# Kernel tuning notes

Hardware: AMD Instinct MI355X
Metric: run time of the kernel (lower is better)

The kernel has to match this reference:

```python
import jax, jax.numpy as jnp
import numpy as np

V = 100000   # nodes (atoms)
E = 400000   # directed edges (bonds x2)
N = 74       # node_feat_size
NE = 12      # edge_feat_size
G = 200      # graph_feat_size
L = 2        # num_layers - 1 GNN layers
OUT = 1      # output_size
NG = 4000    # molecules in the batch


def _lin_init(k, fan_in, fan_out):
    s = 1.0 / np.sqrt(fan_in)
    return jax.random.uniform(k, (fan_in, fan_out), jnp.float32, -s, s)


def setup_inputs() -> dict:
    key = jax.random.key(0)
    ks = list(jax.random.split(key, 40))
    p = {}
    # node feats uniform in (0.05, 0.95) so mask = 1/(sum(h[:,-4:])*(1-h[:,0])) - 1 is finite
    p["node_feats"] = jax.random.uniform(ks[0], (V, N), jnp.float32, 0.05, 0.95)
    p["edge_feats"] = jax.random.normal(ks[1], (E, NE), jnp.float32)
    # GetContext params
    p["pn_W"] = _lin_init(ks[2], N, G);            p["pn_b"] = jnp.zeros((G,), jnp.float32)
    p["pe1_W"] = _lin_init(ks[3], N + NE, G);      p["pe1_b"] = jnp.zeros((G,), jnp.float32)
    p["pe2_W"] = _lin_init(ks[4], 2 * G, 1);       p["pe2_b"] = jnp.zeros((1,), jnp.float32)
    p["et_W"] = _lin_init(ks[5], G, G);            p["et_b"] = jnp.zeros((G,), jnp.float32)
    p["gru0_Wih"] = _lin_init(ks[6], G, 3 * G);    p["gru0_Whh"] = _lin_init(ks[7], G, 3 * G)
    p["gru0_bih"] = jnp.zeros((3 * G,), jnp.float32)
    p["gru0_bhh"] = jnp.zeros((3 * G,), jnp.float32)
    # stacked GNNLayer params
    p["gnn_pe_W"] = jnp.stack([_lin_init(ks[8 + l], 2 * G, 1) for l in range(L)])
    p["gnn_pe_b"] = jnp.zeros((L, 1), jnp.float32)
    p["gnn_pn_W"] = jnp.stack([_lin_init(ks[10 + l], G, G) for l in range(L)])
    p["gnn_pn_b"] = jnp.zeros((L, G), jnp.float32)
    p["gnn_gru_Wih"] = jnp.stack([_lin_init(ks[12 + l], G, 3 * G) for l in range(L)])
    p["gnn_gru_Whh"] = jnp.stack([_lin_init(ks[14 + l], G, 3 * G) for l in range(L)])
    p["gnn_gru_bih"] = jnp.zeros((L, 3 * G), jnp.float32)
    p["gnn_gru_bhh"] = jnp.zeros((L, 3 * G), jnp.float32)
    p["pred_W"] = _lin_init(ks[16], G, OUT);       p["pred_b"] = jnp.zeros((OUT,), jnp.float32)
    # graph structure
    p["src"] = jax.random.randint(ks[17], (E,), 0, V)
    p["dst"] = jax.random.randint(ks[18], (E,), 0, V)
    p["graph_ids"] = jnp.arange(V, dtype=jnp.int32) // (V // NG)  # sorted, balanced, non-empty
    p["n_graphs"] = NG
    return p


def _edge_softmax(logits, dst, num_nodes):
    # softmax over incoming edges of each destination node (DGL edge_softmax)
    m = jax.ops.segment_max(logits, dst, num_segments=num_nodes)
    e = jnp.exp(logits - m[dst])
    s = jax.ops.segment_sum(e, dst, num_segments=num_nodes)
    return e / s[dst]


def _gru_cell(x, h, Wih, Whh, bih, bhh):
    gi = x @ Wih + bih
    gh = h @ Whh + bhh
    ir, iz, inn = jnp.split(gi, 3, axis=-1)
    hr, hz, hn = jnp.split(gh, 3, axis=-1)
    r = jax.nn.sigmoid(ir + hr)
    z = jax.nn.sigmoid(iz + hz)
    n = jnp.tanh(inn + r * hn)
    return (1.0 - z) * n + z * h


def _forward(node_feats, edge_feats, pn_W, pn_b, pe1_W, pe1_b, pe2_W, pe2_b,
             et_W, et_b, gru0_Wih, gru0_Whh, gru0_bih, gru0_bhh,
             gnn_pe_W, gnn_pe_b, gnn_pn_W, gnn_pn_b,
             gnn_gru_Wih, gnn_gru_Whh, gnn_gru_bih, gnn_gru_bhh,
             pred_W, pred_b, src, dst, graph_ids, n_graphs):
    Vn = node_feats.shape[0]
    lrelu = jax.nn.leaky_relu  # slope 0.01, matches torch default
    # mask from original node features g.ndata['h']
    mask = jnp.sum(node_feats[:, -4:], axis=1) * (1.0 - node_feats[:, 0])
    mask = 1.0 / mask - 1.0
    # --- GetContext ---
    hv_new = lrelu(node_feats @ pn_W + pn_b)                               # (V, G)
    he1 = lrelu(jnp.concatenate([node_feats[src], edge_feats], 1) @ pe1_W + pe1_b)  # (E, G)
    he2 = jnp.concatenate([hv_new[dst], he1], 1)                           # (E, 2G)
    logits = lrelu(he2 @ pe2_W + pe2_b)                                    # (E, 1)
    a = _edge_softmax(logits, dst, Vn)
    e = a * (he1 @ et_W + et_b)                                            # (E, G)
    c = jax.ops.segment_sum(e, dst, num_segments=Vn)                       # (V, G)
    nf = jax.nn.relu(_gru_cell(jax.nn.elu(c), hv_new,
                               gru0_Wih, gru0_Whh, gru0_bih, gru0_bhh))
    # --- GNN layers ---
    for l in range(gnn_pe_W.shape[0]):
        he = jnp.concatenate([nf[dst], nf[src]], 1)                        # (E, 2G)
        lg = lrelu(he @ gnn_pe_W[l] + gnn_pe_b[l])                         # (E, 1)
        a = _edge_softmax(lg, dst, Vn)
        hvp = nf @ gnn_pn_W[l] + gnn_pn_b[l]                               # (V, G)
        c = jax.ops.segment_sum(hvp[src] * a, dst, num_segments=Vn)        # (V, G)
        nf = jax.nn.relu(_gru_cell(jax.nn.elu(c), nf,
                                   gnn_gru_Wih[l], gnn_gru_Whh[l],
                                   gnn_gru_bih[l], gnn_gru_bhh[l]))
    # --- readout ---
    atom_pka = nf @ pred_W + pred_b                                        # (V, 1)
    atom_pka = -(atom_pka + mask[:, None])
    h_pow = jnp.power(10.0, atom_pka)
    g_feats = -jnp.log10(jax.ops.segment_sum(h_pow, graph_ids, num_segments=n_graphs))
    atom_pka_out = -atom_pka
    return g_feats, atom_pka_out


def reference(node_feats, edge_feats, pn_W, pn_b, pe1_W, pe1_b, pe2_W, pe2_b,
              et_W, et_b, gru0_Wih, gru0_Whh, gru0_bih, gru0_bhh,
              gnn_pe_W, gnn_pe_b, gnn_pn_W, gnn_pn_b,
              gnn_gru_Wih, gnn_gru_Whh, gnn_gru_bih, gnn_gru_bhh,
              pred_W, pred_b, src, dst, graph_ids, n_graphs):
    return _forward(node_feats, edge_feats, pn_W, pn_b, pe1_W, pe1_b, pe2_W, pe2_b,
                    et_W, et_b, gru0_Wih, gru0_Whh, gru0_bih, gru0_bhh,
                    gnn_pe_W, gnn_pe_b, gnn_pn_W, gnn_pn_b,
                    gnn_gru_Wih, gnn_gru_Whh, gnn_gru_bih, gnn_gru_bhh,
                    pred_W, pred_b, src, dst, graph_ids, n_graphs)
```

## Files before the change

kernel.cpp:

```cpp
#include <hip/hip_runtime.h>
#include <hip/hip_bf16.h>
#include <math.h>

#define V_N    100000
#define E_N    400000
#define NFEAT  74
#define NEFEAT 12
#define G_DIM  200
#define LDA    224
#define L_N    2
#define NG_N   4000
#define NROWB  391
#define NROWP  392
#define NSWZ   (NROWP / 8 * 56)
#define NSWZG  (NROWP / 8 * 112)

static inline int cdiv(int a, int b) { return (a + b - 1) / b; }

__device__ __forceinline__ float lrelu_f(float x) { return x > 0.f ? x : 0.01f * x; }
__device__ __forceinline__ float sigmoid_f(float x) { return 1.f / (1.f + expf(-x)); }
__device__ __forceinline__ float elu_f(float x) { return x > 0.f ? x : expm1f(x); }
__device__ __forceinline__ float bf2f(__hip_bfloat16 x) { return __bfloat162float(x); }
__device__ __forceinline__ float bfbits2f(short s) {
    return __uint_as_float(((unsigned)(unsigned short)s) << 16);
}

__device__ __forceinline__ short f2bf(float f) {
    __hip_bfloat16 b = __float2bfloat16(f);
    short s;
    __builtin_memcpy(&s, &b, 2);
    return s;
}

typedef short short8 __attribute__((ext_vector_type(8)));
typedef short short4v __attribute__((ext_vector_type(4)));
typedef float f32x4 __attribute__((ext_vector_type(4)));

#define MFMA16(a, b, c) __builtin_amdgcn_mfma_f32_16x16x32_bf16((a), (b), (c), 0, 0, 0)

#define GLOAD_LDS16(gp, lp) \
    __builtin_amdgcn_global_load_lds((const __attribute__((address_space(1))) void*)(gp), \
                                     (__attribute__((address_space(3))) void*)(lp), 16, 0, 0)

__device__ __forceinline__ void swz_decode7(int lin, int& rowBlk, int& cb)
{
    int grp = lin / 56;
    int rem = lin % 56;
    cb = rem >> 3;
    rowBlk = grp * 8 + (rem & 7);
}

__device__ __forceinline__ void swz_decode14(int lin, int& rowBlk, int& cb)
{
    int grp = lin / 112;
    int rem = lin % 112;
    cb = rem >> 3;
    rowBlk = grp * 8 + (rem & 7);
}

__device__ __forceinline__ f32x4 qcalc(const f32x4* wef, f32x4 ef0, f32x4 ef1, f32x4 ef2)
{
    f32x4 q = ef0[0] * wef[0];
    q += ef0[1] * wef[1];
    q += ef0[2] * wef[2];
    q += ef0[3] * wef[3];
    q += ef1[0] * wef[4];
    q += ef1[1] * wef[5];
    q += ef1[2] * wef[6];
    q += ef1[3] * wef[7];
    q += ef2[0] * wef[8];
    q += ef2[1] * wef[9];
    q += ef2[2] * wef[10];
    q += ef2[3] * wef[11];
    return q;
}

__global__ __launch_bounds__(256)
void fill_kernel(float* __restrict__ p, float v, int n)
{
    int i = blockIdx.x * blockDim.x + threadIdx.x;
    if (i < n) p[i] = v;
}

__global__ __launch_bounds__(256)
void fill_int_kernel(int* __restrict__ p, int v, int n)
{
    int i = blockIdx.x * blockDim.x + threadIdx.x;
    if (i < n) p[i] = v;
}

__global__ __launch_bounds__(256)
void pad_zero_kernel(short* __restrict__ base, size_t VP)
{
    int idx = blockIdx.x * blockDim.x + threadIdx.x;
    if (idx >= 4 * V_N) return;
    int mat = idx / V_N, row = idx % V_N;
    short* p = base + (size_t)mat * VP + (long)row * LDA + G_DIM;
    short8 z = {};
    *(short8*)(p) = z;
    *(short8*)(p + 8) = z;
    *(short8*)(p + 16) = z;
}

__global__ __launch_bounds__(256)
void wprep_kernel(const float* __restrict__ W, short* __restrict__ Wp, int K, int Kpad)
{
    int idx = blockIdx.x * 256 + threadIdx.x;
    if (idx >= 256 * Kpad) return;
    int j = idx / Kpad, k = idx % Kpad;
    float v = (j < G_DIM && k < K) ? W[(long)k * G_DIM + j] : 0.f;
    Wp[idx] = f2bf(v);
}

__global__ __launch_bounds__(256)
void wprep_tiled_kernel(const float* __restrict__ W, short* __restrict__ Wp)
{
    int idx = blockIdx.x * 256 + threadIdx.x;
    if (idx >= 7 * 7 * 1024) return;
    int cb = idx / (7 * 1024);
    int r = idx % (7 * 1024);
    int st = r / 1024;
    int r2 = r % 1024;
    int cc = r2 / 32, kk = r2 % 32;
    int col = cb * 32 + cc, k = st * 32 + kk;
    float v = (col < G_DIM && k < G_DIM) ? W[(long)k * G_DIM + col] : 0.f;
    Wp[idx] = f2bf(v);
}

__global__ __launch_bounds__(256)
void gru_wprep_kernel(const float* __restrict__ Wih, const float* __restrict__ Whh,
                      short* __restrict__ Wp)
{
    int idx = blockIdx.x * 256 + threadIdx.x;
    if (idx >= 14 * 14 * 1536) return;
    int cb = idx / (14 * 1536);
    int r = idx % (14 * 1536);
    int st = r / 1536;
    int r2 = r % 1536;
    int g = r2 / 512;
    int r3 = r2 % 512;
    int cc = r3 / 32, kk = r3 % 32;
    int col = cb * 16 + cc;
    float v = 0.f;
    if (col < G_DIM) {
        if (st < 7) {
            int k = st * 32 + kk;
            if (k < G_DIM) v = Wih[(long)k * (3 * G_DIM) + g * G_DIM + col];
        } else {
            int k = (st - 7) * 32 + kk;
            if (k < G_DIM) v = Whh[(long)k * (3 * G_DIM) + g * G_DIM + col];
        }
    }
    Wp[idx] = f2bf(v);
}

__global__ __launch_bounds__(256)
void hist_kernel(const int* __restrict__ dst, int* __restrict__ deg)
{
    int e = blockIdx.x * blockDim.x + threadIdx.x;
    if (e >= E_N) return;
    atomicAdd(&deg[dst[e]], 1);
}

__global__ __launch_bounds__(256)
void scan1_kernel(const int* __restrict__ deg, int* __restrict__ rp, int* __restrict__ bsum)
{
    __shared__ int s[256];
    int tid = threadIdx.x;
    int v = blockIdx.x * 256 + tid;
    int x = (v < V_N) ? deg[v] : 0;
    s[tid] = x;
    __syncthreads();
    for (int off = 1; off < 256; off <<= 1) {
        int t = (tid >= off) ? s[tid - off] : 0;
        __syncthreads();
        s[tid] += t;
        __syncthreads();
    }
    if (v < V_N) rp[v] = s[tid] - x;
    if (tid == 255) bsum[blockIdx.x] = s[255];
}

__global__ void scan2_kernel(int* __restrict__ bsum, int* __restrict__ rp, int nb)
{
    if (threadIdx.x != 0 || blockIdx.x != 0) return;
    int acc = 0;
    for (int b = 0; b < nb; b++) { int t = bsum[b]; bsum[b] = acc; acc += t; }
    rp[V_N] = acc;
}

__global__ __launch_bounds__(256)
void scan3_kernel(int* __restrict__ rp, const int* __restrict__ bsum)
{
    int v = blockIdx.x * 256 + threadIdx.x;
    if (v < V_N) rp[v] += bsum[v >> 8];
}

__global__ __launch_bounds__(256)
void csr_fill_kernel(const int* __restrict__ dst, const int* __restrict__ rp,
                     int* __restrict__ cnt, int* __restrict__ perm)
{
    int e = blockIdx.x * blockDim.x + threadIdx.x;
    if (e >= E_N) return;
    int d = dst[e];
    int pos = rp[d] + atomicAdd(&cnt[d], 1);
    perm[pos] = e;
}

__global__ __launch_bounds__(256)
void gemm_f32a_dual_kernel(const float* __restrict__ Af32,
                           const short* __restrict__ Wp1, const float* __restrict__ b1,
                           const short* __restrict__ Wp2, const float* __restrict__ b2,
                           __hip_bfloat16* __restrict__ C1,
                           __hip_bfloat16* __restrict__ C2)
{
    __shared__ short As[64 * 40];
    __shared__ short Bs1[64 * 40];
    __shared__ short Bs2[64 * 40];
    const int tid = threadIdx.x;
    const int lane = tid & 63;
    const int w = tid >> 6;
    const int quad = lane >> 4;
    const int lm = lane & 15;
    const int rowBase = blockIdx.y * 64;
    const int j0 = blockIdx.x * 64;
    const int arow = tid >> 2;
    const int akc = (tid & 3) * 8;
    const int agrow = rowBase + arow;

    f32x4 acc1[4] = {}, acc2[4] = {};

    for (int k0 = 0; k0 < 96; k0 += 32) {
        short8 av = {};
        if (agrow < V_N) {
            int gk = k0 + akc;
            #pragma unroll
            for (int i = 0; i < 8; i++) {
                int kg = gk + i;
                av[i] = (kg < NFEAT) ? f2bf(Af32[(long)agrow * NFEAT + kg]) : (short)0;
            }
        }
        *(short8*)&As[arow * 40 + akc] = av;
        {
            int col = tid >> 2;
            *(short8*)&Bs1[col * 40 + akc] =
                *(const short8*)(Wp1 + (long)(j0 + col) * 96 + k0 + akc);
            *(short8*)&Bs2[col * 40 + akc] =
                *(const short8*)(Wp2 + (long)(j0 + col) * 96 + k0 + akc);
        }
        __syncthreads();
        short8 a = *(short8*)&As[(w * 16 + lm) * 40 + quad * 8];
        #pragma unroll
        for (int nt = 0; nt < 4; nt++) {
            short8 bb1 = *(short8*)&Bs1[(nt * 16 + lm) * 40 + quad * 8];
            short8 bb2 = *(short8*)&Bs2[(nt * 16 + lm) * 40 + quad * 8];
            acc1[nt] = MFMA16(a, bb1, acc1[nt]);
            acc2[nt] = MFMA16(a, bb2, acc2[nt]);
        }
        __syncthreads();
    }

    #pragma unroll
    for (int nt = 0; nt < 4; nt++) {
        int col = j0 + nt * 16 + lm;
        if (col >= G_DIM) continue;
        float bv1 = b1[col], bv2 = b2[col];
        #pragma unroll
        for (int r = 0; r < 4; r++) {
            int grow = rowBase + w * 16 + quad * 4 + r;
            if (grow >= V_N) continue;
            C1[(long)grow * LDA + col] = __float2bfloat16(lrelu_f(acc1[nt][r] + bv1));
            C2[(long)grow * LDA + col] = __float2bfloat16(acc2[nt][r] + bv2);
        }
    }
}

template<int EPI>
__global__ __launch_bounds__(256)
void gemm_bf16a_kernel(const __hip_bfloat16* __restrict__ Abf,
                       const short* __restrict__ Wp,
                       const float* __restrict__ bias,
                       __hip_bfloat16* __restrict__ Cbf)
{
    __shared__ short As[2][256 * 32];
    __shared__ short Bs[2][32 * 32];
    int rowBlk, cb;
    swz_decode7(blockIdx.x, rowBlk, cb);
    if (rowBlk >= NROWB) return;
    const int tid = threadIdx.x;
    const int lane = tid & 63;
    const int w = tid >> 6;
    const int quad = lane >> 4;
    const int lm = lane & 15;
    const int j0 = cb * 32;
    const int rowBase = rowBlk * 256;

    const short* WpB = Wp + (long)cb * (7 * 1024);
    const short* As_g = (const short*)Abf;
    const long aoff = (long)(rowBase + w * 64 + (lane >> 2)) * LDA + (lane & 3) * 8;
    const int boff = w * 512 + lane * 8;

    auto stage = [&](int st, int buf) {
        const int kl = st * 32;
        #pragma unroll
        for (int c = 0; c < 4; c++)
            GLOAD_LDS16(As_g + aoff + (long)c * 16 * LDA + kl,
                        &As[buf][(w * 64 + c * 16) * 32]);
        if (w < 2)
            GLOAD_LDS16(WpB + st * 1024 + boff, &Bs[buf][w * 512]);
    };

    f32x4 acc[4][2] = {};

    stage(0, 0);
    __syncthreads();

    int buf = 0;
    #pragma unroll 1
    for (int st = 0; st < 7; st++) {
        if (st + 1 < 7) stage(st + 1, buf ^ 1);
        short8 b0 = *(short8*)&Bs[buf][(0 * 16 + lm) * 32 + quad * 8];
        short8 b1 = *(short8*)&Bs[buf][(1 * 16 + lm) * 32 + quad * 8];
        #pragma unroll
        for (int rt = 0; rt < 4; rt++) {
            short8 a = *(short8*)&As[buf][(w * 64 + rt * 16 + lm) * 32 + quad * 8];
            acc[rt][0] = MFMA16(a, b0, acc[rt][0]);
            acc[rt][1] = MFMA16(a, b1, acc[rt][1]);
        }
        __syncthreads();
        buf ^= 1;
    }

    #pragma unroll
    for (int nt = 0; nt < 2; nt++) {
        int col = j0 + nt * 16 + lm;
        if (col >= G_DIM) continue;
        float bv = bias[col];
        #pragma unroll
        for (int rt = 0; rt < 4; rt++) {
            #pragma unroll
            for (int r = 0; r < 4; r++) {
                int grow = rowBase + w * 64 + rt * 16 + quad * 4 + r;
                if (grow >= V_N) continue;
                float v = acc[rt][nt][r] + bv;
                if (EPI == 3) v = elu_f(v);
                Cbf[(long)grow * LDA + col] = __float2bfloat16(v);
            }
        }
    }
}

__global__ __launch_bounds__(256, 3)
void gru_mfma_kernel(const __hip_bfloat16* __restrict__ xc,
                     const __hip_bfloat16* __restrict__ h,
                     const short* __restrict__ Wp,
                     const float* __restrict__ bih, const float* __restrict__ bhh,
                     __hip_bfloat16* __restrict__ out)
{
    __shared__ short As[2][256 * 32];
    __shared__ short Bs[2][3 * 16 * 32];
    int rowBlk, cb;
    swz_decode14(blockIdx.x, rowBlk, cb);
    if (rowBlk >= NROWB) return;
    const int tid = threadIdx.x;
    const int lane = tid & 63;
    const int w = tid >> 6;
    const int quad = lane >> 4;
    const int lm = lane & 15;
    const int j0 = cb * 16;
    const int rowBase = rowBlk * 256;

    const short* WpB = Wp + (long)cb * (14 * 1536);
    const short* xc_s = (const short*)xc;
    const short* h_s = (const short*)h;
    const long aoff = (long)(rowBase + w * 64 + (lane >> 2)) * LDA + (lane & 3) * 8;
    const int boff = w * 512 + lane * 8;

    auto stage = [&](int st, int buf) {
        const short* Ap = (st < 7) ? xc_s : h_s;
        const int kl = (st < 7 ? st : st - 7) * 32;
        #pragma unroll
        for (int c = 0; c < 4; c++)
            GLOAD_LDS16(Ap + aoff + (long)c * 16 * LDA + kl,
                        &As[buf][(w * 64 + c * 16) * 32]);
        if (w < 3)
            GLOAD_LDS16(WpB + st * 1536 + boff, &Bs[buf][w * 512]);
    };

    f32x4 aR[4] = {}, aZ[4] = {}, aNl[4] = {}, aNh[4] = {};

    stage(0, 0);
    __syncthreads();

    int buf = 0;
    #pragma unroll 1
    for (int st = 0; st < 14; st++) {
        if (st + 1 < 14) stage(st + 1, buf ^ 1);
        short8 br = *(short8*)&Bs[buf][(0 * 16 + lm) * 32 + quad * 8];
        short8 bz = *(short8*)&Bs[buf][(1 * 16 + lm) * 32 + quad * 8];
        short8 bn = *(short8*)&Bs[buf][(2 * 16 + lm) * 32 + quad * 8];
        #pragma unroll
        for (int rt = 0; rt < 4; rt++) {
            short8 a = *(short8*)&As[buf][(w * 64 + rt * 16 + lm) * 32 + quad * 8];
            aR[rt] = MFMA16(a, br, aR[rt]);
            aZ[rt] = MFMA16(a, bz, aZ[rt]);
            if (st < 7) aNl[rt] = MFMA16(a, bn, aNl[rt]);
            else        aNh[rt] = MFMA16(a, bn, aNh[rt]);
        }
        __syncthreads();
        buf ^= 1;
    }

    int col = j0 + lm;
    if (col < G_DIM) {
        float b_ir = bih[col], b_iz = bih[G_DIM + col], b_in = bih[2 * G_DIM + col];
        float b_hr = bhh[col], b_hz = bhh[G_DIM + col], b_hn = bhh[2 * G_DIM + col];
        #pragma unroll
        for (int rt = 0; rt < 4; rt++) {
            #pragma unroll
            for (int r = 0; r < 4; r++) {
                int grow = rowBase + w * 64 + rt * 16 + quad * 4 + r;
                if (grow >= V_N) continue;
                float sr = aR[rt][r] + b_ir + b_hr;
                float sz = aZ[rt][r] + b_iz + b_hz;
                float gin = aNl[rt][r] + b_in;
                float ghn = aNh[rt][r] + b_hn;
                float rr = sigmoid_f(sr);
                float zz = sigmoid_f(sz);
                float nn = tanhf(gin + rr * ghn);
                float hval = bf2f(h[(long)grow * LDA + col]);
                float o = (1.f - zz) * nn + zz * hval;
                out[(long)grow * LDA + col] = __float2bfloat16(o > 0.f ? o : 0.f);
            }
        }
    }
}

__global__ __launch_bounds__(256)
void node_dot2_kernel(const __hip_bfloat16* __restrict__ X,
                      const float* __restrict__ wa, const float* __restrict__ wb,
                      float* __restrict__ s1, float* __restrict__ s2)
{
    int w = threadIdx.x >> 6, lane = threadIdx.x & 63;
    int v = blockIdx.x * 4 + w;
    if (v >= V_N) return;
    int vlane = (lane < 50) ? lane : 0;
    short4v pv = *(const short4v*)((const short*)X + (long)v * LDA + vlane * 4);
    f32x4 wav = *(const f32x4*)(wa + vlane * 4);
    float a = 0.f, b = 0.f;
    #pragma unroll
    for (int u = 0; u < 4; u++) a += bfbits2f(pv[u]) * wav[u];
    if (wb) {
        f32x4 wbv = *(const f32x4*)(wb + vlane * 4);
        #pragma unroll
        for (int u = 0; u < 4; u++) b += bfbits2f(pv[u]) * wbv[u];
    }
    if (lane >= 50) { a = 0.f; b = 0.f; }
    for (int off = 32; off > 0; off >>= 1) {
        a += __shfl_down(a, off, 64);
        if (wb) b += __shfl_down(b, off, 64);
    }
    if (lane == 0) {
        s1[v] = a;
        if (wb) s2[v] = b;
    }
}

__global__ __launch_bounds__(256)
void ctx_fused_kernel(const __hip_bfloat16* __restrict__ P,
                      const float* __restrict__ efeat,
                      const int* __restrict__ src,
                      const int* __restrict__ rp, const int* __restrict__ perm,
                      const float* __restrict__ s1,
                      const float* __restrict__ pe1W,
                      const float* __restrict__ pe2W, const float* __restrict__ pe2b,
                      __hip_bfloat16* __restrict__ hbar)
{
    const int tid = threadIdx.x;
    const int w = tid >> 6, lane = tid & 63;
    const int vlane = (lane < 50) ? lane : 0;
    const int v = __builtin_amdgcn_readfirstlane(blockIdx.x * 4 + w);
    if (v >= V_N) return;
    const int b = __builtin_amdgcn_readfirstlane(rp[v]);
    const int en = __builtin_amdgcn_readfirstlane(rp[v + 1]);
    if (en == b) {
        if (lane < 50) {
            short4v z = {};
            *(short4v*)((short*)hbar + (long)v * LDA + lane * 4) = z;
        }
        return;
    }
    f32x4 wef[12];
    #pragma unroll
    for (int j = 0; j < 12; j++)
        wef[j] = *(const f32x4*)(pe1W + (long)(NFEAT + j) * G_DIM + vlane * 4);
    const f32x4 w2 = *(const f32x4*)(pe2W + G_DIM + vlane * 4);
    const float s1b = s1[v] + pe2b[0];

    float m = -INFINITY, ssum = 0.f;
    f32x4 a = {};
    for (int i = b; i < en; i++) {
        const int e = __builtin_amdgcn_readfirstlane(perm[i]);
        const int sN = __builtin_amdgcn_readfirstlane(src[e]);
        const f32x4 ef0 = *(const f32x4*)(efeat + (long)e * NEFEAT);
        const f32x4 ef1 = *(const f32x4*)(efeat + (long)e * NEFEAT + 4);
        const f32x4 ef2 = *(const f32x4*)(efeat + (long)e * NEFEAT + 8);
        const short4v pv = *(const short4v*)((const short*)P + (long)sN * LDA + vlane * 4);
        const f32x4 q = qcalc(wef, ef0, ef1, ef2);
        f32x4 he;
        #pragma unroll
        for (int u = 0; u < 4; u++) he[u] = lrelu_f(bfbits2f(pv[u]) + q[u]);
        float dot = he[0] * w2[0] + he[1] * w2[1] + he[2] * w2[2] + he[3] * w2[3];
        if (lane >= 50) dot = 0.f;
        #pragma unroll
        for (int off = 32; off > 0; off >>= 1) dot += __shfl_xor(dot, off, 64);
        const float l = lrelu_f(dot + s1b);
        if (l <= m) {
            const float wgt = expf(l - m);
            ssum += wgt;
            #pragma unroll
            for (int u = 0; u < 4; u++) a[u] += wgt * he[u];
        } else {
            const float scale = expf(m - l);
            ssum = ssum * scale + 1.f;
            #pragma unroll
            for (int u = 0; u < 4; u++) a[u] = a[u] * scale + he[u];
            m = l;
        }
    }
    const float inv = 1.f / ssum;
    if (lane < 50) {
        short4v o;
        #pragma unroll
        for (int u = 0; u < 4; u++) o[u] = f2bf(a[u] * inv);
        *(short4v*)((short*)hbar + (long)v * LDA + lane * 4) = o;
    }
}

__global__ __launch_bounds__(256)
void gnn_fused_agg_kernel(const __hip_bfloat16* __restrict__ X,
                          const int* __restrict__ src,
                          const int* __restrict__ rp, const int* __restrict__ perm,
                          const float* __restrict__ s1, const float* __restrict__ s2,
                          const float* __restrict__ bias,
                          __hip_bfloat16* __restrict__ out)
{
    const int tid = threadIdx.x;
    const int w = tid >> 6, lane = tid & 63;
    const int vlane = (lane < 50) ? lane : 0;
    const int v = __builtin_amdgcn_readfirstlane(blockIdx.x * 4 + w);
    if (v >= V_N) return;
    const int b = __builtin_amdgcn_readfirstlane(rp[v]);
    const int en = __builtin_amdgcn_readfirstlane(rp[v + 1]);
    if (en == b) {
        if (lane < 50) {
            short4v z = {};
            *(short4v*)((short*)out + (long)v * LDA + lane * 4) = z;
        }
        return;
    }
    const float s1v = s1[v] + bias[0];
    float m = -INFINITY;
    for (int i = b; i < en; i++) {
        const int e = __builtin_amdgcn_readfirstlane(perm[i]);
        const int sN = __builtin_amdgcn_readfirstlane(src[e]);
        m = fmaxf(m, lrelu_f(s1v + s2[sN]));
    }
    f32x4 a = {};
    float ssum = 0.f;
    for (int i = b; i < en; i++) {
        const int e = __builtin_amdgcn_readfirstlane(perm[i]);
        const int sN = __builtin_amdgcn_readfirstlane(src[e]);
        const float l = lrelu_f(s1v + s2[sN]);
        const float wgt = expf(l - m);
        ssum += wgt;
        const short4v pv = *(const short4v*)((const short*)X + (long)sN * LDA + vlane * 4);
        #pragma unroll
        for (int u = 0; u < 4; u++)
            a[u] += wgt * bfbits2f(pv[u]);
    }
    const float inv = 1.f / ssum;
    if (lane < 50) {
        short4v o;
        #pragma unroll
        for (int u = 0; u < 4; u++) o[u] = f2bf(elu_f(a[u] * inv));
        *(short4v*)((short*)out + (long)v * LDA + lane * 4) = o;
    }
}

__global__ __launch_bounds__(256)
void mask_kernel(const float* __restrict__ nfeat, float* __restrict__ mask)
{
    int v = blockIdx.x * blockDim.x + threadIdx.x;
    if (v >= V_N) return;
    const float* row = nfeat + (long)v * NFEAT;
    float s = row[NFEAT - 4] + row[NFEAT - 3] + row[NFEAT - 2] + row[NFEAT - 1];
    float m = s * (1.f - row[0]);
    mask[v] = 1.f / m - 1.f;
}

__global__ __launch_bounds__(256)
void readout_kernel(const __hip_bfloat16* __restrict__ nf, const float* __restrict__ predW,
                    const float* __restrict__ predb, const float* __restrict__ mask,
                    const int* __restrict__ gid, float* __restrict__ out_atom,
                    float* __restrict__ gsum)
{
    int gtid = blockIdx.x * blockDim.x + threadIdx.x;
    int v = gtid >> 6, lane = gtid & 63;
    if (v >= V_N) return;
    int vlane = (lane < 50) ? lane : 0;
    short4v pv = *(const short4v*)((const short*)nf + (long)v * LDA + vlane * 4);
    f32x4 wv = *(const f32x4*)(predW + vlane * 4);
    float acc = 0.f;
    #pragma unroll
    for (int u = 0; u < 4; u++) acc += bfbits2f(pv[u]) * wv[u];
    if (lane >= 50) acc = 0.f;
    for (int off = 32; off > 0; off >>= 1) acc += __shfl_down(acc, off, 64);
    if (lane == 0) {
        float p = acc + predb[0] + mask[v];
        out_atom[v] = p;
        atomicAdd(&gsum[gid[v]], exp10f(-p));
    }
}

__global__ __launch_bounds__(256)
void graph_out_kernel(const float* __restrict__ gsum, float* __restrict__ out_g)
{
    int g = blockIdx.x * blockDim.x + threadIdx.x;
    if (g >= NG_N) return;
    out_g[g] = -log10f(gsum[g]);
}

extern "C" void kernel_launch(void* const* d_in, const int* in_sizes, int n_in,
                              void* d_out, int out_size, void* d_ws, size_t ws_size,
                              hipStream_t stream)
{
    const float* node_feats = (const float*)d_in[0];
    const float* edge_feats = (const float*)d_in[1];
    const float* pn_W  = (const float*)d_in[2];
    const float* pn_b  = (const float*)d_in[3];
    const float* pe1_W = (const float*)d_in[4];
    const float* pe1_b = (const float*)d_in[5];
    const float* pe2_W = (const float*)d_in[6];
    const float* pe2_b = (const float*)d_in[7];
    const float* et_W  = (const float*)d_in[8];
    const float* et_b  = (const float*)d_in[9];
    const float* gru0_Wih = (const float*)d_in[10];
    const float* gru0_Whh = (const float*)d_in[11];
    const float* gru0_bih = (const float*)d_in[12];
    const float* gru0_bhh = (const float*)d_in[13];
    const float* gnn_pe_W = (const float*)d_in[14];
    const float* gnn_pe_b = (const float*)d_in[15];
    const float* gnn_pn_W = (const float*)d_in[16];
    const float* gnn_pn_b = (const float*)d_in[17];
    const float* gnn_gru_Wih = (const float*)d_in[18];
    const float* gnn_gru_Whh = (const float*)d_in[19];
    const float* gnn_gru_bih = (const float*)d_in[20];
    const float* gnn_gru_bhh = (const float*)d_in[21];
    const float* pred_W = (const float*)d_in[22];
    const float* pred_b = (const float*)d_in[23];
    const int* src = (const int*)d_in[24];
    const int* dst = (const int*)d_in[25];
    const int* gid = (const int*)d_in[26];

    float* out_g = (float*)d_out;
    float* out_atom = out_g + NG_N;

    char* base = (char*)d_ws;
    size_t off = 0;
    auto take = [&](size_t bytes) -> void* {
        void* p = base + off;
        off += (bytes + 255) & ~(size_t)255;
        return p;
    };
    const size_t VP = (size_t)V_N * LDA;
    const size_t WPL = (size_t)14 * 14 * 1536;
    float* mask   = (float*)take((size_t)V_N * 4);
    float* s1     = (float*)take((size_t)V_N * 4);
    float* s2     = (float*)take((size_t)V_N * 4);
    float* gsum   = (float*)take((size_t)NG_N * 4);
    __hip_bfloat16* c    = (__hip_bfloat16*)take(VP * 2);
    __hip_bfloat16* hv   = (__hip_bfloat16*)take(VP * 2);
    __hip_bfloat16* nf_a = (__hip_bfloat16*)take(VP * 2);
    __hip_bfloat16* nf_b = (__hip_bfloat16*)take(VP * 2);
    short* WpGru = (short*)take(3 * WPL * 2);
    short* Wp_pn0 = (short*)take((size_t)256 * 96 * 2);
    short* Wp_pe1 = (short*)take((size_t)256 * 96 * 2);
    short* Wp_et  = (short*)take((size_t)7 * 7 * 1024 * 2);
    short* Wp_pn1 = (short*)take((size_t)7 * 7 * 1024 * 2);
    short* Wp_pn2 = (short*)take((size_t)7 * 7 * 1024 * 2);
    int* deg  = (int*)take((size_t)V_N * 4);
    int* cnt  = (int*)take((size_t)V_N * 4);
    int* rp   = (int*)take((size_t)(V_N + 1) * 4);
    int* perm = (int*)take((size_t)E_N * 4);
    int* bsum = (int*)take((size_t)512 * 4);
    __hip_bfloat16* P    = nf_a;
    __hip_bfloat16* hbar = nf_b;
    __hip_bfloat16* hvp  = hv;

    if (off > ws_size) {
        fill_kernel<<<cdiv(out_size, 256), 256, 0, stream>>>((float*)d_out, -12345.f, out_size);
        return;
    }

    const int BLK = 256;
    const int nScanBlocks = cdiv(V_N, 256);
    const dim3 gOld(4, cdiv(V_N, 64));
    const int gAgg = cdiv(V_N, 4);

    pad_zero_kernel<<<cdiv(4 * V_N, BLK), BLK, 0, stream>>>((short*)c, VP);

    gru_wprep_kernel<<<cdiv(14 * 14 * 1536, 256), BLK, 0, stream>>>(gru0_Wih, gru0_Whh, WpGru);
    for (int l = 0; l < L_N; l++)
        gru_wprep_kernel<<<cdiv(14 * 14 * 1536, 256), BLK, 0, stream>>>(
            gnn_gru_Wih + (size_t)l * G_DIM * 3 * G_DIM,
            gnn_gru_Whh + (size_t)l * G_DIM * 3 * G_DIM,
            WpGru + (size_t)(l + 1) * WPL);
    wprep_kernel<<<cdiv(256 * 96, 256), BLK, 0, stream>>>(pn_W, Wp_pn0, NFEAT, 96);
    wprep_kernel<<<cdiv(256 * 96, 256), BLK, 0, stream>>>(pe1_W, Wp_pe1, NFEAT, 96);
    wprep_tiled_kernel<<<cdiv(7 * 7 * 1024, 256), BLK, 0, stream>>>(et_W, Wp_et);
    wprep_tiled_kernel<<<cdiv(7 * 7 * 1024, 256), BLK, 0, stream>>>(gnn_pn_W, Wp_pn1);
    wprep_tiled_kernel<<<cdiv(7 * 7 * 1024, 256), BLK, 0, stream>>>(
        gnn_pn_W + (size_t)G_DIM * G_DIM, Wp_pn2);

    mask_kernel<<<cdiv(V_N, BLK), BLK, 0, stream>>>(node_feats, mask);

    fill_int_kernel<<<cdiv(V_N, BLK), BLK, 0, stream>>>(deg, 0, V_N);
    hist_kernel<<<cdiv(E_N, BLK), BLK, 0, stream>>>(dst, deg);
    scan1_kernel<<<nScanBlocks, BLK, 0, stream>>>(deg, rp, bsum);
    scan2_kernel<<<1, 1, 0, stream>>>(bsum, rp, nScanBlocks);
    scan3_kernel<<<nScanBlocks, BLK, 0, stream>>>(rp, bsum);
    fill_int_kernel<<<cdiv(V_N, BLK), BLK, 0, stream>>>(cnt, 0, V_N);
    csr_fill_kernel<<<cdiv(E_N, BLK), BLK, 0, stream>>>(dst, rp, cnt, perm);

    gemm_f32a_dual_kernel<<<gOld, BLK, 0, stream>>>(
        node_feats, Wp_pn0, pn_b, Wp_pe1, pe1_b, hv, P);
    node_dot2_kernel<<<gAgg, BLK, 0, stream>>>(hv, pe2_W, nullptr, s1, nullptr);
    ctx_fused_kernel<<<gAgg, BLK, 0, stream>>>(
        P, edge_feats, src, rp, perm, s1, pe1_W, pe2_W, pe2_b, hbar);
    gemm_bf16a_kernel<3><<<NSWZ, BLK, 0, stream>>>(hbar, Wp_et, et_b, c);
    gru_mfma_kernel<<<NSWZG, BLK, 0, stream>>>(c, hv, WpGru, gru0_bih, gru0_bhh, nf_a);

    __hip_bfloat16* cur = nf_a;
    __hip_bfloat16* nxt = nf_b;
    for (int l = 0; l < L_N; l++) {
        const float* pe_W = gnn_pe_W + (size_t)l * 2 * G_DIM;
        const float* pe_b = gnn_pe_b + l;
        const float* pnB  = gnn_pn_b + (size_t)l * G_DIM;
        const float* bih  = gnn_gru_bih + (size_t)l * 3 * G_DIM;
        const float* bhh  = gnn_gru_bhh + (size_t)l * 3 * G_DIM;
        const short* WpPn = (l == 0) ? Wp_pn1 : Wp_pn2;

        node_dot2_kernel<<<gAgg, BLK, 0, stream>>>(cur, pe_W, pe_W + G_DIM, s1, s2);
        gemm_bf16a_kernel<1><<<NSWZ, BLK, 0, stream>>>(cur, WpPn, pnB, hvp);
        gnn_fused_agg_kernel<<<gAgg, BLK, 0, stream>>>(
            hvp, src, rp, perm, s1, s2, pe_b, c);
        gru_mfma_kernel<<<NSWZG, BLK, 0, stream>>>(
            c, cur, WpGru + (size_t)(l + 1) * WPL, bih, bhh, nxt);

        __hip_bfloat16* tmp = cur; cur = nxt; nxt = tmp;
    }

    fill_kernel<<<cdiv(NG_N, BLK), BLK, 0, stream>>>(gsum, 0.f, NG_N);
    readout_kernel<<<cdiv(V_N * 64, BLK), BLK, 0, stream>>>(
        cur, pred_W, pred_b, mask, gid, out_atom, gsum);
    graph_out_kernel<<<cdiv(NG_N, BLK), BLK, 0, stream>>>(gsum, out_g);
}
```

Before: 1.227 ms.

## Load GEMM and GRU operands directly into registers instead of staging through LDS

The dense GEMM and GRU MFMA kernels no longer stage A and B tiles through shared memory with global_load_lds and barriers. Each lane now loads its MFMA fragments straight from global memory into registers, prefetching the next k-step while the current one computes. The GRU kernel also drops its occupancy hint from launch_bounds. This removes the LDS traffic and the __syncthreads barriers, but each wave now issues its own global loads for shared B fragments, and the loads are strided row-wise with less coalescing. Register pressure also rises.

```diff
diff --git a/kernel.cpp b/kernel.cpp
--- a/kernel.cpp
+++ b/kernel.cpp
@@ -37,10 +37,6 @@
 typedef float f32x4 __attribute__((ext_vector_type(4)));
 
 #define MFMA16(a, b, c) __builtin_amdgcn_mfma_f32_16x16x32_bf16((a), (b), (c), 0, 0, 0)
-
-#define GLOAD_LDS16(gp, lp) \
-    __builtin_amdgcn_global_load_lds((const __attribute__((address_space(1))) void*)(gp), \
-                                     (__attribute__((address_space(3))) void*)(lp), 16, 0, 0)
 
 __device__ __forceinline__ void swz_decode7(int lin, int& rowBlk, int& cb)
 {
@@ -282,8 +278,6 @@
                        const float* __restrict__ bias,
                        __hip_bfloat16* __restrict__ Cbf)
 {
-    __shared__ short As[2][256 * 32];
-    __shared__ short Bs[2][32 * 32];
     int rowBlk, cb;
     swz_decode7(blockIdx.x, rowBlk, cb);
     if (rowBlk >= NROWB) return;
@@ -297,38 +291,44 @@
 
     const short* WpB = Wp + (long)cb * (7 * 1024);
     const short* As_g = (const short*)Abf;
-    const long aoff = (long)(rowBase + w * 64 + (lane >> 2)) * LDA + (lane & 3) * 8;
-    const int boff = w * 512 + lane * 8;
-
-    auto stage = [&](int st, int buf) {
-        const int kl = st * 32;
-        #pragma unroll
-        for (int c = 0; c < 4; c++)
-            GLOAD_LDS16(As_g + aoff + (long)c * 16 * LDA + kl,
-                        &As[buf][(w * 64 + c * 16) * 32]);
-        if (w < 2)
-            GLOAD_LDS16(WpB + st * 1024 + boff, &Bs[buf][w * 512]);
+    const long abase = (long)(rowBase + w * 64 + lm) * LDA + quad * 8;
+    const int bbase = lm * 32 + quad * 8;
+
+    auto loadA = [&](int st, short8 af[4]) {
+        #pragma unroll
+        for (int rt = 0; rt < 4; rt++)
+            af[rt] = *(const short8*)(As_g + abase + (long)rt * 16 * LDA + st * 32);
     };
+    auto loadB = [&](int st, short8 bf[2]) {
+        const short* bp = WpB + st * 1024 + bbase;
+        #pragma unroll
+        for (int nt = 0; nt < 2; nt++)
+            bf[nt] = *(const short8*)(bp + nt * 512);
+    };
 
     f32x4 acc[4][2] = {};
-
-    stage(0, 0);
-    __syncthreads();
-
-    int buf = 0;
+    short8 aF[4], bF[2];
+    loadA(0, aF);
+    loadB(0, bF);
+
     #pragma unroll 1
     for (int st = 0; st < 7; st++) {
-        if (st + 1 < 7) stage(st + 1, buf ^ 1);
-        short8 b0 = *(short8*)&Bs[buf][(0 * 16 + lm) * 32 + quad * 8];
-        short8 b1 = *(short8*)&Bs[buf][(1 * 16 + lm) * 32 + quad * 8];
+        short8 aN[4], bN[2];
+        if (st + 1 < 7) {
+            loadA(st + 1, aN);
+            loadB(st + 1, bN);
+        }
         #pragma unroll
         for (int rt = 0; rt < 4; rt++) {
-            short8 a = *(short8*)&As[buf][(w * 64 + rt * 16 + lm) * 32 + quad * 8];
-            acc[rt][0] = MFMA16(a, b0, acc[rt][0]);
-            acc[rt][1] = MFMA16(a, b1, acc[rt][1]);
-        }
-        __syncthreads();
-        buf ^= 1;
+            acc[rt][0] = MFMA16(aF[rt], bF[0], acc[rt][0]);
+            acc[rt][1] = MFMA16(aF[rt], bF[1], acc[rt][1]);
+        }
+        if (st + 1 < 7) {
+            #pragma unroll
+            for (int rt = 0; rt < 4; rt++) aF[rt] = aN[rt];
+            bF[0] = bN[0];
+            bF[1] = bN[1];
+        }
     }
 
     #pragma unroll
@@ -350,15 +350,13 @@
     }
 }
 
-__global__ __launch_bounds__(256, 3)
+__global__ __launch_bounds__(256)
 void gru_mfma_kernel(const __hip_bfloat16* __restrict__ xc,
                      const __hip_bfloat16* __restrict__ h,
                      const short* __restrict__ Wp,
                      const float* __restrict__ bih, const float* __restrict__ bhh,
                      __hip_bfloat16* __restrict__ out)
 {
-    __shared__ short As[2][256 * 32];
-    __shared__ short Bs[2][3 * 16 * 32];
     int rowBlk, cb;
     swz_decode14(blockIdx.x, rowBlk, cb);
     if (rowBlk >= NROWB) return;
@@ -373,42 +371,52 @@
     const short* WpB = Wp + (long)cb * (14 * 1536);
     const short* xc_s = (const short*)xc;
     const short* h_s = (const short*)h;
-    const long aoff = (long)(rowBase + w * 64 + (lane >> 2)) * LDA + (lane & 3) * 8;
-    const int boff = w * 512 + lane * 8;
-
-    auto stage = [&](int st, int buf) {
-        const short* Ap = (st < 7) ? xc_s : h_s;
-        const int kl = (st < 7 ? st : st - 7) * 32;
-        #pragma unroll
-        for (int c = 0; c < 4; c++)
-            GLOAD_LDS16(Ap + aoff + (long)c * 16 * LDA + kl,
-                        &As[buf][(w * 64 + c * 16) * 32]);
-        if (w < 3)
-            GLOAD_LDS16(WpB + st * 1536 + boff, &Bs[buf][w * 512]);
+    const long abase = (long)(rowBase + w * 64 + lm) * LDA + quad * 8;
+    const int bbase = lm * 32 + quad * 8;
+
+    auto loadA = [&](const short* Ap, int kst, short8 af[4]) {
+        #pragma unroll
+        for (int rt = 0; rt < 4; rt++)
+            af[rt] = *(const short8*)(Ap + abase + (long)rt * 16 * LDA + kst * 32);
     };
+    auto loadB = [&](int st, short8 bf[3]) {
+        const short* bp = WpB + st * 1536 + bbase;
+        #pragma unroll
+        for (int g = 0; g < 3; g++)
+            bf[g] = *(const short8*)(bp + g * 512);
+    };
 
     f32x4 aR[4] = {}, aZ[4] = {}, aNl[4] = {}, aNh[4] = {};
-
-    stage(0, 0);
-    __syncthreads();
-
-    int buf = 0;
+    short8 aF[4], bF[3];
+    loadA(xc_s, 0, aF);
+    loadB(0, bF);
+
     #pragma unroll 1
     for (int st = 0; st < 14; st++) {
-        if (st + 1 < 14) stage(st + 1, buf ^ 1);
-        short8 br = *(short8*)&Bs[buf][(0 * 16 + lm) * 32 + quad * 8];
-        short8 bz = *(short8*)&Bs[buf][(1 * 16 + lm) * 32 + quad * 8];
-        short8 bn = *(short8*)&Bs[buf][(2 * 16 + lm) * 32 + quad * 8];
+        short8 aN[4], bN[3];
+        if (st + 1 < 14) {
+            const short* Ap = (st + 1 < 7) ? xc_s : h_s;
+            loadA(Ap, (st + 1 < 7) ? st + 1 : st - 6, aN);
+            loadB(st + 1, bN);
+        }
         #pragma unroll
         for (int rt = 0; rt < 4; rt++) {
-            short8 a = *(short8*)&As[buf][(w * 64 + rt * 16 + lm) * 32 + quad * 8];
-            aR[rt] = MFMA16(a, br, aR[rt]);
-            aZ[rt] = MFMA16(a, bz, aZ[rt]);
-            if (st < 7) aNl[rt] = MFMA16(a, bn, aNl[rt]);
-            else        aNh[rt] = MFMA16(a, bn, aNh[rt]);
-        }
-        __syncthreads();
-        buf ^= 1;
+            aR[rt] = MFMA16(aF[rt], bF[0], aR[rt]);
+            aZ[rt] = MFMA16(aF[rt], bF[1], aZ[rt]);
+        }
+        if (st < 7) {
+            #pragma unroll
+            for (int rt = 0; rt < 4; rt++) aNl[rt] = MFMA16(aF[rt], bF[2], aNl[rt]);
+        } else {
+            #pragma unroll
+            for (int rt = 0; rt < 4; rt++) aNh[rt] = MFMA16(aF[rt], bF[2], aNh[rt]);
+        }
+        if (st + 1 < 14) {
+            #pragma unroll
+            for (int rt = 0; rt < 4; rt++) aF[rt] = aN[rt];
+            #pragma unroll
+            for (int g = 0; g < 3; g++) bF[g] = bN[g];
+        }
     }
 
     int col = j0 + lm;
```

After: 1.399 ms. 1.14x slower.
